# Optimization experiments

Measured on AMD Instinct MI355X. Metric: run time of the kernel, lower is better.

The kernel has to match this reference:

```python
import jax, jax.numpy as jnp
import numpy as np

N, C_IN, C_INNER, K = 2_000_000, 20, 20, 9
EPS = 1e-5


def _bn(y, gamma, beta):
    # BatchNorm1d forward with batch statistics (torch training-mode forward, biased var)
    m = jnp.mean(y, axis=0)
    v = jnp.mean((y - m) ** 2, axis=0)
    return (y - m) * jax.lax.rsqrt(v + EPS) * gamma + beta


def setup_inputs() -> dict:
    key = jax.random.key(0)
    ks = jax.random.split(key, 8)
    feature = jax.random.normal(ks[0], (N, C_IN), dtype=jnp.float32)
    index = jax.random.randint(ks[1], (N, K), 0, N, dtype=jnp.int32)
    s1 = 1.0 / np.sqrt(C_IN)
    s3 = 1.0 / np.sqrt(C_IN + C_INNER)
    return {
        "feature": feature,
        "index": index,
        "W1": jax.random.uniform(ks[2], (C_IN, C_INNER), jnp.float32, -s1, s1),
        "b1": jax.random.uniform(ks[3], (C_INNER,), jnp.float32, -s1, s1),
        "g1": jnp.ones((C_INNER,), jnp.float32),
        "be1": jnp.zeros((C_INNER,), jnp.float32),
        "g2": jnp.ones((C_INNER,), jnp.float32),
        "be2": jnp.zeros((C_INNER,), jnp.float32),
        "W3": jax.random.uniform(ks[4], (C_IN + C_INNER, C_INNER), jnp.float32, -s3, s3),
        "b3": jax.random.uniform(ks[5], (C_INNER,), jnp.float32, -s3, s3),
        "g3": jnp.ones((C_INNER,), jnp.float32),
        "be3": jnp.zeros((C_INNER,), jnp.float32),
    }


def reference(feature, index, W1, b1, g1, be1, g2, be2, W3, b3, g3, be3):
    # x = BN(Linear(feature))  [N, C]
    x = _bn(feature @ W1 + b1, g1, be1)
    idx = index.astype(jnp.int32)
    xg = x[idx]                                   # [N, K, C] neighbor gather
    w = jax.nn.softmax(jnp.einsum('nc,nkc->nk', x, xg), axis=1)  # attention weights
    out = jnp.einsum('nk,nkc->nc', w, xg)         # weighted aggregation (pass 1)
    out = jnp.einsum('nk,nkc->nc', w, out[idx])   # repeat > 1: second pass with same weights
    out = jnp.concatenate([jax.nn.relu(_bn(out, g2, be2)), feature], axis=1)  # [N, C_IN+C_INNER]
    return jax.nn.relu(_bn(out @ W3 + b3, g3, be3))
```

## Files before the change

### kernel.cpp

```cpp
#include <hip/hip_runtime.h>
#include <hip/hip_bf16.h>
#include <math.h>

#define N_ROWS 2000000
#define C 20
#define K 9
#define EPS 1e-5f

#define GRID_RED 2048
#define BLK 256


__device__ inline float wave_sum(float v) {
    v += __shfl_xor(v, 1);
    v += __shfl_xor(v, 2);
    v += __shfl_xor(v, 4);
    v += __shfl_xor(v, 8);
    v += __shfl_xor(v, 16);
    v += __shfl_xor(v, 32);
    return v;
}

__device__ inline void block_reduce_partials(float* vals, float* __restrict__ partials) {
    __shared__ float sred[BLK / 64][2 * C];
    const int lane = threadIdx.x & 63;
    const int wid = threadIdx.x >> 6;
#pragma unroll
    for (int i = 0; i < 2 * C; i++) vals[i] = wave_sum(vals[i]);
    if (lane == 0) {
#pragma unroll
        for (int i = 0; i < 2 * C; i++) sred[wid][i] = vals[i];
    }
    __syncthreads();
    if (threadIdx.x < 2 * C) {
        float s = 0.f;
#pragma unroll
        for (int w = 0; w < BLK / 64; w++) s += sred[w][threadIdx.x];
        partials[(size_t)blockIdx.x * (2 * C) + threadIdx.x] = s;
    }
}

__device__ inline void load_row20(const float* __restrict__ p, float* v) {
    const float4* q = (const float4*)p;
#pragma unroll
    for (int i = 0; i < 5; i++) {
        float4 t = q[i];
        v[4 * i + 0] = t.x; v[4 * i + 1] = t.y; v[4 * i + 2] = t.z; v[4 * i + 3] = t.w;
    }
}

__device__ inline void store_row20(float* __restrict__ p, const float* v) {
    float4* q = (float4*)p;
#pragma unroll
    for (int i = 0; i < 5; i++) {
        float4 t;
        t.x = v[4 * i + 0]; t.y = v[4 * i + 1]; t.z = v[4 * i + 2]; t.w = v[4 * i + 3];
        q[i] = t;
    }
}


__global__ __launch_bounds__(BLK) void kA(const float* __restrict__ feat,
                                          const float* __restrict__ W1,
                                          const float* __restrict__ b1,
                                          float* __restrict__ y1,
                                          float* __restrict__ partials) {
    float sums[2 * C];
#pragma unroll
    for (int i = 0; i < 2 * C; i++) sums[i] = 0.f;

    for (int r = blockIdx.x * BLK + threadIdx.x; r < N_ROWS; r += GRID_RED * BLK) {
        float f[C];
        load_row20(feat + (size_t)r * C, f);
        float y[C];
#pragma unroll
        for (int c = 0; c < C; c++) y[c] = b1[c];
#pragma unroll
        for (int i = 0; i < C; i++) {
            float fi = f[i];
#pragma unroll
            for (int c = 0; c < C; c++) y[c] = fmaf(fi, W1[i * C + c], y[c]);
        }
        store_row20(y1 + (size_t)r * C, y);
#pragma unroll
        for (int c = 0; c < C; c++) {
            sums[c] += y[c];
            sums[C + c] = fmaf(y[c], y[c], sums[C + c]);
        }
    }
    block_reduce_partials(sums, partials);
}


__global__ __launch_bounds__(640) void kFin(const float* __restrict__ partials,
                                            const float* __restrict__ g,
                                            const float* __restrict__ be,
                                            float* __restrict__ ss) {
    const int c = threadIdx.x >> 4;
    const int r = threadIdx.x & 15;
    __shared__ float tot[2 * C];
    {
        float s = 0.f;
        for (int b = r; b < GRID_RED; b += 16) s += partials[(size_t)b * (2 * C) + c];
        s += __shfl_xor(s, 1);
        s += __shfl_xor(s, 2);
        s += __shfl_xor(s, 4);
        s += __shfl_xor(s, 8);
        if (r == 0) tot[c] = s;
    }
    __syncthreads();
    if (threadIdx.x < C) {
        const int cc = threadIdx.x;
        const float invN = 1.0f / (float)N_ROWS;
        float mean = tot[cc] * invN;
        float var = tot[C + cc] * invN - mean * mean;
        float scale = g[cc] * rsqrtf(var + EPS);
        ss[cc] = scale;
        ss[C + cc] = be[cc] - mean * scale;
    }
}


__global__ __launch_bounds__(BLK) void kC(const float* __restrict__ y1,
                                          const int* __restrict__ index,
                                          const float* __restrict__ ss1,
                                          float* __restrict__ out,
                                          float* __restrict__ wbuf) {
    const int n = blockIdx.x * BLK + threadIdx.x;
    if (n >= N_ROWS) return;

    float sc[C], sh[C];
#pragma unroll
    for (int c = 0; c < C; c++) { sc[c] = ss1[c]; sh[c] = ss1[C + c]; }

    float x[C];
    {
        float t[C];
        load_row20(y1 + (size_t)n * C, t);
#pragma unroll
        for (int c = 0; c < C; c++) x[c] = fmaf(t[c], sc[c], sh[c]);
    }

    int idx[K];
#pragma unroll
    for (int k = 0; k < K; k++) idx[k] = index[(size_t)n * K + k];

    float m = -INFINITY, l = 0.f;
    float acc[C];
    float s[K];
#pragma unroll
    for (int c = 0; c < C; c++) acc[c] = 0.f;

#pragma unroll
    for (int k = 0; k < K; k++) {
        float gch[C];
        {
            float t[C];
            load_row20(y1 + (size_t)idx[k] * C, t);
#pragma unroll
            for (int c = 0; c < C; c++) gch[c] = fmaf(t[c], sc[c], sh[c]);
        }
        float d0 = 0.f, d1 = 0.f;
#pragma unroll
        for (int c = 0; c < C; c += 2) {
            d0 = fmaf(x[c], gch[c], d0);
            d1 = fmaf(x[c + 1], gch[c + 1], d1);
        }
        const float dot = d0 + d1;
        s[k] = dot;
        const float mn = fmaxf(m, dot);
        const float rr = __expf(m - mn);
        const float pp = __expf(dot - mn);
        l = fmaf(l, rr, pp);
#pragma unroll
        for (int c = 0; c < C; c++) acc[c] = fmaf(acc[c], rr, pp * gch[c]);
        m = mn;
    }

    const float linv = 1.f / l;
    float o[C];
#pragma unroll
    for (int c = 0; c < C; c++) o[c] = acc[c] * linv;
    store_row20(out + (size_t)n * C, o);
#pragma unroll
    for (int k = 0; k < K; k++) wbuf[(size_t)n * K + k] = __expf(s[k] - m) * linv;
}


__global__ __launch_bounds__(BLK) void kD(const float* __restrict__ out,
                                          const int* __restrict__ index,
                                          const float* __restrict__ wbuf,
                                          float* __restrict__ out2,
                                          float* __restrict__ partials) {
    float sums[2 * C];
#pragma unroll
    for (int i = 0; i < 2 * C; i++) sums[i] = 0.f;

    for (int n = blockIdx.x * BLK + threadIdx.x; n < N_ROWS; n += GRID_RED * BLK) {
        float wv[K];
        int idx[K];
#pragma unroll
        for (int k = 0; k < K; k++) {
            wv[k] = wbuf[(size_t)n * K + k];
            idx[k] = index[(size_t)n * K + k];
        }
        float acc[C];
#pragma unroll
        for (int c = 0; c < C; c++) acc[c] = 0.f;
#pragma unroll
        for (int k = 0; k < K; k++) {
            float t[C];
            load_row20(out + (size_t)idx[k] * C, t);
#pragma unroll
            for (int c = 0; c < C; c++) acc[c] = fmaf(wv[k], t[c], acc[c]);
        }
        store_row20(out2 + (size_t)n * C, acc);
#pragma unroll
        for (int c = 0; c < C; c++) {
            sums[c] += acc[c];
            sums[C + c] = fmaf(acc[c], acc[c], sums[C + c]);
        }
    }
    block_reduce_partials(sums, partials);
}


__global__ __launch_bounds__(BLK) void kF(const float* __restrict__ feat,
                                          const float* __restrict__ W3,
                                          const float* __restrict__ b3,
                                          const float* __restrict__ ss2,
                                          float* __restrict__ zio,
                                          float* __restrict__ partials) {
    float sums[2 * C];
#pragma unroll
    for (int i = 0; i < 2 * C; i++) sums[i] = 0.f;

    for (int n = blockIdx.x * BLK + threadIdx.x; n < N_ROWS; n += GRID_RED * BLK) {
        float h[2 * C];
        {
            float t[C];
            load_row20(zio + (size_t)n * C, t);
#pragma unroll
            for (int c = 0; c < C; c++) h[c] = fmaxf(0.f, fmaf(t[c], ss2[c], ss2[C + c]));
        }
        load_row20(feat + (size_t)n * C, h + C);

        float z[C];
#pragma unroll
        for (int c = 0; c < C; c++) z[c] = b3[c];
#pragma unroll
        for (int i = 0; i < 2 * C; i++) {
            float hi = h[i];
#pragma unroll
            for (int c = 0; c < C; c++) z[c] = fmaf(hi, W3[i * C + c], z[c]);
        }
        store_row20(zio + (size_t)n * C, z);
#pragma unroll
        for (int c = 0; c < C; c++) {
            sums[c] += z[c];
            sums[C + c] = fmaf(z[c], z[c], sums[C + c]);
        }
    }
    block_reduce_partials(sums, partials);
}


__global__ __launch_bounds__(BLK) void kH(const float* __restrict__ z,
                                          const float* __restrict__ ss3,
                                          float* __restrict__ outF) {
    for (int n = blockIdx.x * BLK + threadIdx.x; n < N_ROWS; n += GRID_RED * BLK) {
        float t[C];
        load_row20(z + (size_t)n * C, t);
        float o[C];
#pragma unroll
        for (int c = 0; c < C; c++) o[c] = fmaxf(0.f, fmaf(t[c], ss3[c], ss3[C + c]));
        store_row20(outF + (size_t)n * C, o);
    }
}


extern "C" void kernel_launch(void* const* d_in, const int* in_sizes, int n_in,
                              void* d_out, int out_size, void* d_ws, size_t ws_size,
                              hipStream_t stream) {
    const float* feature = (const float*)d_in[0];
    const int* index = (const int*)d_in[1];
    const float* W1 = (const float*)d_in[2];
    const float* b1 = (const float*)d_in[3];
    const float* g1 = (const float*)d_in[4];
    const float* be1 = (const float*)d_in[5];
    const float* g2 = (const float*)d_in[6];
    const float* be2 = (const float*)d_in[7];
    const float* W3 = (const float*)d_in[8];
    const float* b3 = (const float*)d_in[9];
    const float* g3 = (const float*)d_in[10];
    const float* be3 = (const float*)d_in[11];
    float* outp = (float*)d_out;

    float* B0 = (float*)d_ws;
    float* B1 = B0 + (size_t)N_ROWS * C;
    float* partials = B1 + (size_t)N_ROWS * K;
    float* ss1 = partials + (size_t)GRID_RED * (2 * C);
    float* ss2 = ss1 + 2 * C;
    float* ss3 = ss2 + 2 * C;

    const int gridC = (N_ROWS + BLK - 1) / BLK;

    kA<<<GRID_RED, BLK, 0, stream>>>(feature, W1, b1, B0, partials);
    kFin<<<1, 640, 0, stream>>>(partials, g1, be1, ss1);
    kC<<<gridC, BLK, 0, stream>>>(B0, index, ss1, outp, B1);
    kD<<<GRID_RED, BLK, 0, stream>>>(outp, index, B1, B0, partials);
    kFin<<<1, 640, 0, stream>>>(partials, g2, be2, ss2);
    kF<<<GRID_RED, BLK, 0, stream>>>(feature, W3, b3, ss2, B0, partials);
    kFin<<<1, 640, 0, stream>>>(partials, g3, be3, ss3);
    kH<<<GRID_RED, BLK, 0, stream>>>(B0, ss3, outp);
}
```

Baseline: 2.430 ms.

## Store gathered activations as fp16 padded rows, recompute linear, use nontemporal accesses

Stores the normalized activations and first-pass aggregation as fp16 rows padded to 64 bytes, so each random neighbor gather reads one aligned 64B segment instead of 80B of fp32. The first linear layer is recomputed in a new kernel kB instead of writing and re-reading y1. The attention weight buffer becomes column-major, and streaming accesses use nontemporal loads and stores. It also adds occupancy hints in launch bounds and reuses the output buffer in place. The fp16 storage loses precision in the attention scores and aggregation, which may affect numerical tolerance.

```diff
diff --git a/kernel.cpp b/kernel.cpp
--- a/kernel.cpp
+++ b/kernel.cpp
@@ -1,6 +1,7 @@
 #include <hip/hip_runtime.h>
-#include <hip/hip_bf16.h>
+#include <hip/hip_fp16.h>
 #include <math.h>
+#include <string.h>
 
 #define N_ROWS 2000000
 #define C 20
@@ -9,6 +10,92 @@
 
 #define GRID_RED 2048
 #define BLK 256
+
+typedef float f32x4 __attribute__((ext_vector_type(4)));
+typedef unsigned int u32x4 __attribute__((ext_vector_type(4)));
+typedef unsigned int u32x2 __attribute__((ext_vector_type(2)));
+
+template <typename T> __device__ inline T ntl(const T* p) { return __builtin_nontemporal_load(p); }
+template <typename T> __device__ inline void nts(T* p, T v) { __builtin_nontemporal_store(v, p); }
+
+
+__device__ inline unsigned int pk2(float a, float b) {
+    __half2 h = __floats2half2_rn(a, b);
+    unsigned int u;
+    memcpy(&u, &h, 4);
+    return u;
+}
+
+__device__ inline void upk2(unsigned int u, float& a, float& b) {
+    __half2 h;
+    memcpy(&h, &u, 4);
+    float2 f = __half22float2(h);
+    a = f.x;
+    b = f.y;
+}
+
+template <int RPU>
+__device__ inline void load_row_h(const unsigned int* __restrict__ p, float* v) {
+    unsigned int u[10];
+    if constexpr (RPU == 16) {
+        u32x4 a = *(const u32x4*)p;
+        u32x4 b = *(const u32x4*)(p + 4);
+        u32x2 c = *(const u32x2*)(p + 8);
+        u[0] = a.x; u[1] = a.y; u[2] = a.z; u[3] = a.w;
+        u[4] = b.x; u[5] = b.y; u[6] = b.z; u[7] = b.w;
+        u[8] = c.x; u[9] = c.y;
+    } else {
+#pragma unroll
+        for (int i = 0; i < 5; i++) {
+            u32x2 t = *(const u32x2*)(p + 2 * i);
+            u[2 * i] = t.x;
+            u[2 * i + 1] = t.y;
+        }
+    }
+#pragma unroll
+    for (int i = 0; i < 10; i++) upk2(u[i], v[2 * i], v[2 * i + 1]);
+}
+
+template <int RPU>
+__device__ inline void store_row_h(unsigned int* __restrict__ p, const float* v) {
+    unsigned int u[10];
+#pragma unroll
+    for (int i = 0; i < 10; i++) u[i] = pk2(v[2 * i], v[2 * i + 1]);
+    if constexpr (RPU == 16) {
+        u32x4 a; a.x = u[0]; a.y = u[1]; a.z = u[2]; a.w = u[3];
+        u32x4 b; b.x = u[4]; b.y = u[5]; b.z = u[6]; b.w = u[7];
+        u32x2 c; c.x = u[8]; c.y = u[9];
+        *(u32x4*)p = a;
+        *(u32x4*)(p + 4) = b;
+        *(u32x2*)(p + 8) = c;
+    } else {
+#pragma unroll
+        for (int i = 0; i < 5; i++) {
+            u32x2 t; t.x = u[2 * i]; t.y = u[2 * i + 1];
+            *(u32x2*)(p + 2 * i) = t;
+        }
+    }
+}
+
+
+__device__ inline void load_row20_nt(const float* __restrict__ p, float* v) {
+    const f32x4* q = (const f32x4*)p;
+#pragma unroll
+    for (int i = 0; i < 5; i++) {
+        f32x4 t = ntl(q + i);
+        v[4 * i + 0] = t.x; v[4 * i + 1] = t.y; v[4 * i + 2] = t.z; v[4 * i + 3] = t.w;
+    }
+}
+
+__device__ inline void store_row20_nt(float* __restrict__ p, const float* v) {
+    f32x4* q = (f32x4*)p;
+#pragma unroll
+    for (int i = 0; i < 5; i++) {
+        f32x4 t;
+        t.x = v[4 * i + 0]; t.y = v[4 * i + 1]; t.z = v[4 * i + 2]; t.w = v[4 * i + 3];
+        nts(q + i, t);
+    }
+}
 
 
 __device__ inline float wave_sum(float v) {
@@ -40,38 +127,18 @@
     }
 }
 
-__device__ inline void load_row20(const float* __restrict__ p, float* v) {
-    const float4* q = (const float4*)p;
-#pragma unroll
-    for (int i = 0; i < 5; i++) {
-        float4 t = q[i];
-        v[4 * i + 0] = t.x; v[4 * i + 1] = t.y; v[4 * i + 2] = t.z; v[4 * i + 3] = t.w;
-    }
-}
-
-__device__ inline void store_row20(float* __restrict__ p, const float* v) {
-    float4* q = (float4*)p;
-#pragma unroll
-    for (int i = 0; i < 5; i++) {
-        float4 t;
-        t.x = v[4 * i + 0]; t.y = v[4 * i + 1]; t.z = v[4 * i + 2]; t.w = v[4 * i + 3];
-        q[i] = t;
-    }
-}
-
-
-__global__ __launch_bounds__(BLK) void kA(const float* __restrict__ feat,
-                                          const float* __restrict__ W1,
-                                          const float* __restrict__ b1,
-                                          float* __restrict__ y1,
-                                          float* __restrict__ partials) {
+
+__global__ __launch_bounds__(BLK, 3) void kA(const float* __restrict__ feat,
+                                             const float* __restrict__ W1,
+                                             const float* __restrict__ b1,
+                                             float* __restrict__ partials) {
     float sums[2 * C];
 #pragma unroll
     for (int i = 0; i < 2 * C; i++) sums[i] = 0.f;
 
     for (int r = blockIdx.x * BLK + threadIdx.x; r < N_ROWS; r += GRID_RED * BLK) {
         float f[C];
-        load_row20(feat + (size_t)r * C, f);
+        load_row20_nt(feat + (size_t)r * C, f);
         float y[C];
 #pragma unroll
         for (int c = 0; c < C; c++) y[c] = b1[c];
@@ -81,7 +148,6 @@
 #pragma unroll
             for (int c = 0; c < C; c++) y[c] = fmaf(fi, W1[i * C + c], y[c]);
         }
-        store_row20(y1 + (size_t)r * C, y);
 #pragma unroll
         for (int c = 0; c < C; c++) {
             sums[c] += y[c];
@@ -121,29 +187,46 @@
 }
 
 
-__global__ __launch_bounds__(BLK) void kC(const float* __restrict__ y1,
-                                          const int* __restrict__ index,
-                                          const float* __restrict__ ss1,
-                                          float* __restrict__ out,
-                                          float* __restrict__ wbuf) {
+template <int RPU>
+__global__ __launch_bounds__(BLK, 4) void kB(const float* __restrict__ feat,
+                                             const float* __restrict__ W1,
+                                             const float* __restrict__ b1,
+                                             const float* __restrict__ ss1,
+                                             unsigned int* __restrict__ xh) {
     const int n = blockIdx.x * BLK + threadIdx.x;
     if (n >= N_ROWS) return;
-
-    float sc[C], sh[C];
-#pragma unroll
-    for (int c = 0; c < C; c++) { sc[c] = ss1[c]; sh[c] = ss1[C + c]; }
-
+    float f[C];
+    load_row20_nt(feat + (size_t)n * C, f);
+    float y[C];
+#pragma unroll
+    for (int c = 0; c < C; c++) y[c] = b1[c];
+#pragma unroll
+    for (int i = 0; i < C; i++) {
+        float fi = f[i];
+#pragma unroll
+        for (int c = 0; c < C; c++) y[c] = fmaf(fi, W1[i * C + c], y[c]);
+    }
     float x[C];
-    {
-        float t[C];
-        load_row20(y1 + (size_t)n * C, t);
-#pragma unroll
-        for (int c = 0; c < C; c++) x[c] = fmaf(t[c], sc[c], sh[c]);
-    }
+#pragma unroll
+    for (int c = 0; c < C; c++) x[c] = fmaf(y[c], ss1[c], ss1[C + c]);
+    store_row_h<RPU>(xh + (size_t)n * RPU, x);
+}
+
+
+template <int RPU>
+__global__ __launch_bounds__(BLK, 4) void kC(const unsigned int* __restrict__ xh,
+                                             const int* __restrict__ index,
+                                             float* __restrict__ wbuf,
+                                             unsigned int* __restrict__ oh) {
+    const int n = blockIdx.x * BLK + threadIdx.x;
+    if (n >= N_ROWS) return;
+
+    float x[C];
+    load_row_h<RPU>(xh + (size_t)n * RPU, x);
 
     int idx[K];
 #pragma unroll
-    for (int k = 0; k < K; k++) idx[k] = index[(size_t)n * K + k];
+    for (int k = 0; k < K; k++) idx[k] = ntl(index + (size_t)n * K + k);
 
     float m = -INFINITY, l = 0.f;
     float acc[C];
@@ -154,12 +237,7 @@
 #pragma unroll
     for (int k = 0; k < K; k++) {
         float gch[C];
-        {
-            float t[C];
-            load_row20(y1 + (size_t)idx[k] * C, t);
-#pragma unroll
-            for (int c = 0; c < C; c++) gch[c] = fmaf(t[c], sc[c], sh[c]);
-        }
+        load_row_h<RPU>(xh + (size_t)idx[k] * RPU, gch);
         float d0 = 0.f, d1 = 0.f;
 #pragma unroll
         for (int c = 0; c < C; c += 2) {
@@ -181,17 +259,18 @@
     float o[C];
 #pragma unroll
     for (int c = 0; c < C; c++) o[c] = acc[c] * linv;
-    store_row20(out + (size_t)n * C, o);
-#pragma unroll
-    for (int k = 0; k < K; k++) wbuf[(size_t)n * K + k] = __expf(s[k] - m) * linv;
-}
-
-
-__global__ __launch_bounds__(BLK) void kD(const float* __restrict__ out,
-                                          const int* __restrict__ index,
-                                          const float* __restrict__ wbuf,
-                                          float* __restrict__ out2,
-                                          float* __restrict__ partials) {
+    store_row_h<RPU>(oh + (size_t)n * RPU, o);
+#pragma unroll
+    for (int k = 0; k < K; k++) nts(wbuf + (size_t)k * N_ROWS + n, __expf(s[k] - m) * linv);
+}
+
+
+template <int RPU>
+__global__ __launch_bounds__(BLK, 3) void kD(const unsigned int* __restrict__ oh,
+                                             const int* __restrict__ index,
+                                             const float* __restrict__ wbuf,
+                                             float* __restrict__ out2,
+                                             float* __restrict__ partials) {
     float sums[2 * C];
 #pragma unroll
     for (int i = 0; i < 2 * C; i++) sums[i] = 0.f;
@@ -201,8 +280,8 @@
         int idx[K];
 #pragma unroll
         for (int k = 0; k < K; k++) {
-            wv[k] = wbuf[(size_t)n * K + k];
-            idx[k] = index[(size_t)n * K + k];
+            wv[k] = ntl(wbuf + (size_t)k * N_ROWS + n);
+            idx[k] = ntl(index + (size_t)n * K + k);
         }
         float acc[C];
 #pragma unroll
@@ -210,11 +289,11 @@
 #pragma unroll
         for (int k = 0; k < K; k++) {
             float t[C];
-            load_row20(out + (size_t)idx[k] * C, t);
+            load_row_h<RPU>(oh + (size_t)idx[k] * RPU, t);
 #pragma unroll
             for (int c = 0; c < C; c++) acc[c] = fmaf(wv[k], t[c], acc[c]);
         }
-        store_row20(out2 + (size_t)n * C, acc);
+        store_row20_nt(out2 + (size_t)n * C, acc);
 #pragma unroll
         for (int c = 0; c < C; c++) {
             sums[c] += acc[c];
@@ -225,12 +304,12 @@
 }
 
 
-__global__ __launch_bounds__(BLK) void kF(const float* __restrict__ feat,
-                                          const float* __restrict__ W3,
-                                          const float* __restrict__ b3,
-                                          const float* __restrict__ ss2,
-                                          float* __restrict__ zio,
-                                          float* __restrict__ partials) {
+__global__ __launch_bounds__(BLK, 3) void kF(const float* __restrict__ feat,
+                                             const float* __restrict__ W3,
+                                             const float* __restrict__ b3,
+                                             const float* __restrict__ ss2,
+                                             float* __restrict__ zio,
+                                             float* __restrict__ partials) {
     float sums[2 * C];
 #pragma unroll
     for (int i = 0; i < 2 * C; i++) sums[i] = 0.f;
@@ -239,11 +318,11 @@
         float h[2 * C];
         {
             float t[C];
-            load_row20(zio + (size_t)n * C, t);
+            load_row20_nt(zio + (size_t)n * C, t);
 #pragma unroll
             for (int c = 0; c < C; c++) h[c] = fmaxf(0.f, fmaf(t[c], ss2[c], ss2[C + c]));
         }
-        load_row20(feat + (size_t)n * C, h + C);
+        load_row20_nt(feat + (size_t)n * C, h + C);
 
         float z[C];
 #pragma unroll
@@ -254,7 +333,7 @@
 #pragma unroll
             for (int c = 0; c < C; c++) z[c] = fmaf(hi, W3[i * C + c], z[c]);
         }
-        store_row20(zio + (size_t)n * C, z);
+        store_row20_nt(zio + (size_t)n * C, z);
 #pragma unroll
         for (int c = 0; c < C; c++) {
             sums[c] += z[c];
@@ -265,19 +344,45 @@
 }
 
 
-__global__ __launch_bounds__(BLK) void kH(const float* __restrict__ z,
-                                          const float* __restrict__ ss3,
-                                          float* __restrict__ outF) {
+__global__ __launch_bounds__(BLK, 4) void kH(float* __restrict__ zio,
+                                             const float* __restrict__ ss3) {
     for (int n = blockIdx.x * BLK + threadIdx.x; n < N_ROWS; n += GRID_RED * BLK) {
         float t[C];
-        load_row20(z + (size_t)n * C, t);
+        load_row20_nt(zio + (size_t)n * C, t);
         float o[C];
 #pragma unroll
         for (int c = 0; c < C; c++) o[c] = fmaxf(0.f, fmaf(t[c], ss3[c], ss3[C + c]));
-        store_row20(outF + (size_t)n * C, o);
-    }
-}
-
+        store_row20_nt(zio + (size_t)n * C, o);
+    }
+}
+
+
+template <int RPU>
+static void launch_all(const float* feature, const int* index, const float* W1,
+                       const float* b1, const float* g1, const float* be1,
+                       const float* g2, const float* be2, const float* W3,
+                       const float* b3, const float* g3, const float* be3,
+                       float* outp, void* d_ws, hipStream_t stream) {
+    unsigned int* xh = (unsigned int*)d_ws;
+    unsigned int* oh = xh + (size_t)N_ROWS * RPU;
+    float* wbuf = (float*)(oh + (size_t)N_ROWS * RPU);
+    float* partials = wbuf + (size_t)N_ROWS * K;
+    float* ss1 = partials + (size_t)GRID_RED * (2 * C);
+    float* ss2 = ss1 + 2 * C;
+    float* ss3 = ss2 + 2 * C;
+
+    const int gridR = (N_ROWS + BLK - 1) / BLK;
+
+    kA<<<GRID_RED, BLK, 0, stream>>>(feature, W1, b1, partials);
+    kFin<<<1, 640, 0, stream>>>(partials, g1, be1, ss1);
+    kB<RPU><<<gridR, BLK, 0, stream>>>(feature, W1, b1, ss1, xh);
+    kC<RPU><<<gridR, BLK, 0, stream>>>(xh, index, wbuf, oh);
+    kD<RPU><<<GRID_RED, BLK, 0, stream>>>(oh, index, wbuf, outp, partials);
+    kFin<<<1, 640, 0, stream>>>(partials, g2, be2, ss2);
+    kF<<<GRID_RED, BLK, 0, stream>>>(feature, W3, b3, ss2, outp, partials);
+    kFin<<<1, 640, 0, stream>>>(partials, g3, be3, ss3);
+    kH<<<GRID_RED, BLK, 0, stream>>>(outp, ss3);
+}
 
 extern "C" void kernel_launch(void* const* d_in, const int* in_sizes, int n_in,
                               void* d_out, int out_size, void* d_ws, size_t ws_size,
@@ -296,21 +401,14 @@
     const float* be3 = (const float*)d_in[11];
     float* outp = (float*)d_out;
 
-    float* B0 = (float*)d_ws;
-    float* B1 = B0 + (size_t)N_ROWS * C;
-    float* partials = B1 + (size_t)N_ROWS * K;
-    float* ss1 = partials + (size_t)GRID_RED * (2 * C);
-    float* ss2 = ss1 + 2 * C;
-    float* ss3 = ss2 + 2 * C;
-
-    const int gridC = (N_ROWS + BLK - 1) / BLK;
-
-    kA<<<GRID_RED, BLK, 0, stream>>>(feature, W1, b1, B0, partials);
-    kFin<<<1, 640, 0, stream>>>(partials, g1, be1, ss1);
-    kC<<<gridC, BLK, 0, stream>>>(B0, index, ss1, outp, B1);
-    kD<<<GRID_RED, BLK, 0, stream>>>(outp, index, B1, B0, partials);
-    kFin<<<1, 640, 0, stream>>>(partials, g2, be2, ss2);
-    kF<<<GRID_RED, BLK, 0, stream>>>(feature, W3, b3, ss2, B0, partials);
-    kFin<<<1, 640, 0, stream>>>(partials, g3, be3, ss3);
-    kH<<<GRID_RED, BLK, 0, stream>>>(B0, ss3, outp);
-}
+    const size_t need32 = (size_t)N_ROWS * 16 * 4 * 2 + (size_t)N_ROWS * K * 4 +
+                          (size_t)GRID_RED * (2 * C) * 4 + 6 * C * 4 + 1024;
+
+    if (ws_size >= need32) {
+        launch_all<16>(feature, index, W1, b1, g1, be1, g2, be2, W3, b3, g3, be3,
+                       outp, d_ws, stream);
+    } else {
+        launch_all<10>(feature, index, W1, b1, g1, be1, g2, be2, W3, b3, g3, be3,
+                       outp, d_ws, stream);
+    }
+}
```

Measured after the change: 2.502 ms. +3.0%, slower.
